# Optimization experiments

Measured on AMD Instinct MI355X. Metric: run time of the kernel, lower is better.

The kernel has to match this reference:

```python
import jax, jax.numpy as jnp
import numpy as np

# dMoE config (matches init_kwargs): D=1024, GLU ffn F=2816 (int(2*4096/3) rounded up to 256),
# E=8 experts, top_k=2, erf-GELU activation, normalize_expert_weights=0 (skip), bias added to output.
D = 1024
F = 2816
E = 8
TOP_K = 2


def setup_inputs() -> dict:
    key = jax.random.key(0)
    ks = jax.random.split(key, 6)
    std = 0.02
    x = jax.random.normal(ks[0], (2, 2048, D), dtype=jnp.float32)
    router_w = jax.random.normal(ks[1], (D, E), dtype=jnp.float32) * std
    w1 = jax.random.normal(ks[2], (E, D, F), dtype=jnp.float32) * std
    v1 = jax.random.normal(ks[3], (E, D, F), dtype=jnp.float32) * std
    w2 = jax.random.normal(ks[4], (E, F, D), dtype=jnp.float32) * std
    bias = jnp.zeros((D,), dtype=jnp.float32)
    return {"x": x, "router_w": router_w, "w1": w1, "v1": v1, "w2": w2, "bias": bias}


def reference(x, router_w, w1, v1, w2, bias):
    B, S, d = x.shape
    xt = x.reshape(B * S, d)                       # [T, D] tokens
    # Router: linear -> softmax over experts -> top-k (no weight renormalization, p=0).
    scores = jax.nn.softmax(xt @ router_w, axis=-1)          # [T, E]
    expert_weights, expert_idx = jax.lax.top_k(scores, TOP_K)  # [T, k]
    # Dropless MoE == dense per-expert GLU MLP combined with top-k weights
    # (non-selected experts get weight 0, mathematically identical to dispatch/combine).
    h = jax.nn.gelu(jnp.einsum('td,edf->tef', xt, w1), approximate=False) \
        * jnp.einsum('td,edf->tef', xt, v1)                   # [T, E, F]
    y = jnp.einsum('tef,efd->ted', h, w2)                     # [T, E, D]
    yk = jnp.take_along_axis(y, expert_idx[:, :, None], axis=1)  # [T, k, D]
    out = jnp.sum(expert_weights[:, :, None] * yk, axis=1) + bias
    return out.reshape(B, S, d)
```

## Files before the change

kernel.cpp:

```cpp
#include <hip/hip_runtime.h>
#include <hip/hip_bf16.h>
#include <math.h>

#define D_DIM 1024
#define F_DIM 2816
#define E_NUM 8

#define BM 128
#define BK 64

typedef __attribute__((ext_vector_type(4))) float f32x4;
typedef __attribute__((ext_vector_type(8))) short short8;

__device__ __forceinline__ unsigned short f2bf(float f) {
    unsigned u = __float_as_uint(f);
    u = (u + 0x7FFFu + ((u >> 16) & 1u)) >> 16;
    return (unsigned short)u;
}

__device__ __forceinline__ float gelu_erf(float z) {
    return 0.5f * z * (1.0f + erff(z * 0.70710678118654752f));
}

__device__ __forceinline__ int swz(int row, int kb) {
    return row * 128 + (kb ^ ((row & 7) << 4));
}

__device__ __forceinline__ uint4 pack8(const unsigned short* h) {
    uint4 r;
    r.x = (unsigned)h[0] | ((unsigned)h[1] << 16);
    r.y = (unsigned)h[2] | ((unsigned)h[3] << 16);
    r.z = (unsigned)h[4] | ((unsigned)h[5] << 16);
    r.w = (unsigned)h[6] | ((unsigned)h[7] << 16);
    return r;
}

__device__ __forceinline__ void gload16(const void* g, void* l) {
    __builtin_amdgcn_global_load_lds(
        (const __attribute__((address_space(1))) unsigned int*)g,
        (__attribute__((address_space(3))) unsigned int*)l,
        16, 0, 0);
}

__global__ __launch_bounds__(256) void transpose_cvt2_kernel(
    const float* __restrict__ srcA, unsigned short* __restrict__ dstA,
    const float* __restrict__ srcB, unsigned short* __restrict__ dstB,
    int R, int C)
{
    __shared__ float tile[64][65];
    int z = blockIdx.z;
    const float* s = (z < E_NUM ? srcA : srcB);
    unsigned short* d = (z < E_NUM ? dstA : dstB);
    int e = z & 7;
    s += (size_t)e * R * C;
    d += (size_t)e * R * C;
    int c0 = blockIdx.x * 64;
    int r0 = blockIdx.y * 64;
    int tid = threadIdx.x;
#pragma unroll
    for (int i = 0; i < 4; ++i) {
        int idx = tid + 256 * i;
        int r = idx >> 4, cc = (idx & 15) * 4;
        float4 v = *(const float4*)(s + (size_t)(r0 + r) * C + c0 + cc);
        tile[r][cc] = v.x; tile[r][cc + 1] = v.y; tile[r][cc + 2] = v.z; tile[r][cc + 3] = v.w;
    }
    __syncthreads();
#pragma unroll
    for (int i = 0; i < 2; ++i) {
        int idx = tid + 256 * i;
        int c = idx >> 3, rr = (idx & 7) * 8;
        unsigned short h[8];
#pragma unroll
        for (int j = 0; j < 8; ++j) h[j] = f2bf(tile[rr + j][c]);
        *(uint4*)(d + (size_t)(c0 + c) * R + r0 + rr) = pack8(h);
    }
}

__global__ __launch_bounds__(256) void transpose_cvt_kernel(
    const float* __restrict__ src, unsigned short* __restrict__ dst, int R, int C)
{
    __shared__ float tile[64][65];
    int e = blockIdx.z;
    const float* s = src + (size_t)e * R * C;
    unsigned short* d = dst + (size_t)e * R * C;
    int c0 = blockIdx.x * 64;
    int r0 = blockIdx.y * 64;
    int tid = threadIdx.x;
#pragma unroll
    for (int i = 0; i < 4; ++i) {
        int idx = tid + 256 * i;
        int r = idx >> 4, cc = (idx & 15) * 4;
        float4 v = *(const float4*)(s + (size_t)(r0 + r) * C + c0 + cc);
        tile[r][cc] = v.x; tile[r][cc + 1] = v.y; tile[r][cc + 2] = v.z; tile[r][cc + 3] = v.w;
    }
    __syncthreads();
#pragma unroll
    for (int i = 0; i < 2; ++i) {
        int idx = tid + 256 * i;
        int c = idx >> 3, rr = (idx & 7) * 8;
        unsigned short h[8];
#pragma unroll
        for (int j = 0; j < 8; ++j) h[j] = f2bf(tile[rr + j][c]);
        *(uint4*)(d + (size_t)(c0 + c) * R + r0 + rr) = pack8(h);
    }
}

__global__ __launch_bounds__(64) void router_kernel(
    const float* __restrict__ x, const float* __restrict__ rw,
    unsigned short* __restrict__ xbf, int* __restrict__ tk_idx,
    float* __restrict__ tk_w, int* __restrict__ counts)
{
    int t = blockIdx.x;
    int lane = threadIdx.x;
    const float* xr = x + (size_t)t * D_DIM;
    float acc[E_NUM];
#pragma unroll
    for (int e = 0; e < E_NUM; ++e) acc[e] = 0.f;
#pragma unroll
    for (int i = 0; i < D_DIM / 64; ++i) {
        int d = lane + 64 * i;
        float xv = xr[d];
        xbf[(size_t)t * D_DIM + d] = f2bf(xv);
        const float* rp = rw + (size_t)d * E_NUM;
#pragma unroll
        for (int e = 0; e < E_NUM; ++e) acc[e] += xv * rp[e];
    }
#pragma unroll
    for (int e = 0; e < E_NUM; ++e) {
#pragma unroll
        for (int s = 32; s > 0; s >>= 1) acc[e] += __shfl_xor(acc[e], s, 64);
    }
    float mx = acc[0];
#pragma unroll
    for (int e = 1; e < E_NUM; ++e) mx = fmaxf(mx, acc[e]);
    float p[E_NUM], se = 0.f;
#pragma unroll
    for (int e = 0; e < E_NUM; ++e) { p[e] = expf(acc[e] - mx); se += p[e]; }
    float inv = 1.f / se;
    int e1 = 0;
#pragma unroll
    for (int e = 1; e < E_NUM; ++e) if (p[e] > p[e1]) e1 = e;
    int e2 = (e1 == 0) ? 1 : 0;
#pragma unroll
    for (int e = 0; e < E_NUM; ++e) if (e != e1 && p[e] > p[e2]) e2 = e;
    if (lane == 0) {
        tk_idx[2 * t] = e1; tk_idx[2 * t + 1] = e2;
        tk_w[2 * t] = p[e1] * inv; tk_w[2 * t + 1] = p[e2] * inv;
        atomicAdd(&counts[e1], 1);
        atomicAdd(&counts[e2], 1);
    }
}

__global__ void scan_kernel(const int* __restrict__ counts, int* __restrict__ offsets,
                            int* __restrict__ cursor,
                            int* __restrict__ tile_e, int* __restrict__ tile_row,
                            int* __restrict__ n_mt)
{
    if (threadIdx.x != 0) return;
    int off = 0, nt = 0;
    for (int e = 0; e < E_NUM; ++e) {
        offsets[e] = off;
        cursor[e] = off;
        int ne = counts[e];
        int nti = (ne + BM - 1) / BM;
        for (int i = 0; i < nti; ++i) { tile_e[nt] = e; tile_row[nt] = off + i * BM; ++nt; }
        off += ne;
    }
    offsets[E_NUM] = off;
    *n_mt = nt;
}

__global__ __launch_bounds__(256) void assign_kernel(
    const int* __restrict__ tk_idx, int* __restrict__ cursor,
    int* __restrict__ pair_token, int* __restrict__ pair_pos, int T)
{
    int t = blockIdx.x * 256 + threadIdx.x;
    if (t >= T) return;
#pragma unroll
    for (int s = 0; s < 2; ++s) {
        int e = tk_idx[2 * t + s];
        int pos = atomicAdd(&cursor[e], 1);
        pair_token[pos] = t;
        pair_pos[2 * t + s] = pos;
    }
}

__global__ __launch_bounds__(512) void gemm1_glu_kernel(
    const unsigned short* __restrict__ xbf,
    const unsigned short* __restrict__ w1t, const unsigned short* __restrict__ v1t,
    const int* __restrict__ pair_token, const int* __restrict__ offsets,
    const int* __restrict__ tile_e, const int* __restrict__ tile_row,
    const int* __restrict__ n_mt,
    unsigned short* __restrict__ hbf)
{
    __shared__ __align__(16) unsigned short As[BM * BK];
    __shared__ __align__(16) unsigned short Bs[256 * BK];

    int flat = blockIdx.x + gridDim.x * blockIdx.y;
    int nwg = gridDim.x * gridDim.y;
    int L = (flat & 7) * (nwg >> 3) + (flat >> 3);
    int mt = L % gridDim.x;
    int strip = L / gridDim.x;
    if (mt >= *n_mt) return;
    int e = tile_e[mt];
    int row0 = tile_row[mt];
    int end = offsets[e + 1];
    int n0 = strip * 128;

    int tid = threadIdx.x;
    int lane = tid & 63;
    int wid = tid >> 6;
    int wr = wid >> 2, wc = wid & 3;
    int sub = lane >> 3;
    int srcoff = (((lane & 7) ^ sub) << 4);

    const unsigned short* W0 = w1t + (size_t)e * D_DIM * F_DIM;
    const unsigned short* W1 = v1t + (size_t)e * D_DIM * F_DIM;

    const char* aptr[2];
#pragma unroll
    for (int i = 0; i < 2; ++i) {
        int r = (wid * 2 + i) * 8 + sub;
        int p = row0 + r;
        if (p >= end) p = end - 1;
        aptr[i] = (const char*)(xbf + (size_t)pair_token[p] * D_DIM) + srcoff;
    }
    const char* bptr[4];
#pragma unroll
    for (int i = 0; i < 4; ++i) {
        int r = (wid * 4 + i) * 8 + sub;
        int s = (r >> 5) & 1;
        int col = n0 + (r >> 6) * 32 + (r & 31);
        const unsigned short* base = s ? W1 : W0;
        bptr[i] = (const char*)(base + (size_t)col * D_DIM) + srcoff;
    }

    f32x4 acc[4][4];
#pragma unroll
    for (int m = 0; m < 4; ++m)
#pragma unroll
        for (int n = 0; n < 4; ++n) acc[m][n] = (f32x4){0.f, 0.f, 0.f, 0.f};

    auto STAGE = [&]() {
#pragma unroll
        for (int i = 0; i < 2; ++i) {
            gload16(aptr[i], (char*)As + (wid * 2 + i) * 1024);
            aptr[i] += 128;
        }
#pragma unroll
        for (int i = 0; i < 4; ++i) {
            gload16(bptr[i], (char*)Bs + (wid * 4 + i) * 1024);
            bptr[i] += 128;
        }
    };

    const int NT = D_DIM / BK;
    for (int kt = 0; kt < NT; ++kt) {
        STAGE();
        __syncthreads();
#pragma unroll
        for (int kk = 0; kk < 2; ++kk) {
            int kb = kk * 64 + (lane >> 4) * 16;
            short8 af[4], bf[4];
#pragma unroll
            for (int m = 0; m < 4; ++m) {
                int row = wr * 64 + m * 16 + (lane & 15);
                af[m] = *(const short8*)((char*)As + swz(row, kb));
            }
#pragma unroll
            for (int n = 0; n < 4; ++n) {
                int rn = wc * 64 + n * 16 + (lane & 15);
                bf[n] = *(const short8*)((char*)Bs + swz(rn, kb));
            }
#pragma unroll
            for (int m = 0; m < 4; ++m)
#pragma unroll
                for (int n = 0; n < 4; ++n)
                    acc[m][n] = __builtin_amdgcn_mfma_f32_16x16x32_bf16(af[m], bf[n], acc[m][n], 0, 0, 0);
        }
        __syncthreads();
    }
#pragma unroll
    for (int m = 0; m < 4; ++m) {
#pragma unroll
        for (int j = 0; j < 4; ++j) {
            int rl = wr * 64 + m * 16 + (lane >> 4) * 4 + j;
            int p = row0 + rl;
            if (p < end) {
#pragma unroll
                for (int n = 0; n < 2; ++n) {
                    float z1 = acc[m][n][j];
                    float z2 = acc[m][n + 2][j];
                    int col = n0 + wc * 32 + n * 16 + (lane & 15);
                    hbf[(size_t)p * F_DIM + col] = f2bf(gelu_erf(z1) * z2);
                }
            }
        }
    }
}

__global__ __launch_bounds__(512) void gemm2_kernel(
    const unsigned short* __restrict__ hbf,
    const unsigned short* __restrict__ w2t,
    const int* __restrict__ offsets,
    const int* __restrict__ tile_e, const int* __restrict__ tile_row,
    const int* __restrict__ n_mt,
    float* __restrict__ ypair)
{
    __shared__ __align__(16) unsigned short As[BM * BK];
    __shared__ __align__(16) unsigned short Bs[256 * BK];

    int flat = blockIdx.x + gridDim.x * blockIdx.y;
    int nwg = gridDim.x * gridDim.y;
    int L = (flat & 7) * (nwg >> 3) + (flat >> 3);
    int mt = L % gridDim.x;
    int strip = L / gridDim.x;
    if (mt >= *n_mt) return;
    int e = tile_e[mt];
    int row0 = tile_row[mt];
    int end = offsets[e + 1];
    int n0 = strip * 256;

    int tid = threadIdx.x;
    int lane = tid & 63;
    int wid = tid >> 6;
    int wr = wid >> 2, wc = wid & 3;
    int sub = lane >> 3;
    int srcoff = (((lane & 7) ^ sub) << 4);

    const unsigned short* W = w2t + (size_t)e * D_DIM * F_DIM;

    const char* aptr[2];
#pragma unroll
    for (int i = 0; i < 2; ++i) {
        int r = (wid * 2 + i) * 8 + sub;
        int p = row0 + r;
        if (p >= end) p = end - 1;
        aptr[i] = (const char*)(hbf + (size_t)p * F_DIM) + srcoff;
    }
    const char* bptr[4];
#pragma unroll
    for (int i = 0; i < 4; ++i) {
        int n = (wid * 4 + i) * 8 + sub;
        bptr[i] = (const char*)(W + (size_t)(n0 + n) * F_DIM) + srcoff;
    }

    f32x4 acc[4][4];
#pragma unroll
    for (int m = 0; m < 4; ++m)
#pragma unroll
        for (int n = 0; n < 4; ++n) acc[m][n] = (f32x4){0.f, 0.f, 0.f, 0.f};

    auto STAGE = [&]() {
#pragma unroll
        for (int i = 0; i < 2; ++i) {
            gload16(aptr[i], (char*)As + (wid * 2 + i) * 1024);
            aptr[i] += 128;
        }
#pragma unroll
        for (int i = 0; i < 4; ++i) {
            gload16(bptr[i], (char*)Bs + (wid * 4 + i) * 1024);
            bptr[i] += 128;
        }
    };

    const int NT = F_DIM / BK;
    for (int kt = 0; kt < NT; ++kt) {
        STAGE();
        __syncthreads();
#pragma unroll
        for (int kk = 0; kk < 2; ++kk) {
            int kb = kk * 64 + (lane >> 4) * 16;
            short8 af[4], bf[4];
#pragma unroll
            for (int m = 0; m < 4; ++m) {
                int row = wr * 64 + m * 16 + (lane & 15);
                af[m] = *(const short8*)((char*)As + swz(row, kb));
            }
#pragma unroll
            for (int n = 0; n < 4; ++n) {
                int rn = wc * 64 + n * 16 + (lane & 15);
                bf[n] = *(const short8*)((char*)Bs + swz(rn, kb));
            }
#pragma unroll
            for (int m = 0; m < 4; ++m)
#pragma unroll
                for (int n = 0; n < 4; ++n)
                    acc[m][n] = __builtin_amdgcn_mfma_f32_16x16x32_bf16(af[m], bf[n], acc[m][n], 0, 0, 0);
        }
        __syncthreads();
    }
#pragma unroll
    for (int m = 0; m < 4; ++m) {
#pragma unroll
        for (int j = 0; j < 4; ++j) {
            int rl = wr * 64 + m * 16 + (lane >> 4) * 4 + j;
            int p = row0 + rl;
            if (p < end) {
#pragma unroll
                for (int n = 0; n < 4; ++n)
                    ypair[(size_t)p * D_DIM + n0 + wc * 64 + n * 16 + (lane & 15)] = acc[m][n][j];
            }
        }
    }
}

__global__ __launch_bounds__(256) void combine_kernel(
    const float* __restrict__ ypair, const int* __restrict__ pair_pos,
    const float* __restrict__ tk_w, const float* __restrict__ bias,
    float* __restrict__ out, int total)
{
    int idx = blockIdx.x * 256 + threadIdx.x;
    if (idx >= total) return;
    int t = idx >> 10;
    int d = idx & (D_DIM - 1);
    int p0 = pair_pos[2 * t], p1 = pair_pos[2 * t + 1];
    float r = bias[d] + tk_w[2 * t] * ypair[(size_t)p0 * D_DIM + d]
                      + tk_w[2 * t + 1] * ypair[(size_t)p1 * D_DIM + d];
    out[idx] = r;
}

__global__ void ws_too_small_kernel(float* out, int n) {
    int i = blockIdx.x * 256 + threadIdx.x;
    if (i < n) out[i] = 12345.0f;
}

extern "C" void kernel_launch(void* const* d_in, const int* in_sizes, int n_in,
                              void* d_out, int out_size, void* d_ws, size_t ws_size,
                              hipStream_t stream) {
    const float* x    = (const float*)d_in[0];
    const float* rw   = (const float*)d_in[1];
    const float* w1   = (const float*)d_in[2];
    const float* v1   = (const float*)d_in[3];
    const float* w2   = (const float*)d_in[4];
    const float* bias = (const float*)d_in[5];
    float* out = (float*)d_out;

    int T = in_sizes[0] / D_DIM;
    int P = 2 * T;
    int maxMT = P / BM + E_NUM;

    char* p = (char*)d_ws;
    char* ws_end = p + ws_size;
    auto alloc = [&](size_t bytes) {
        char* r = p;
        p += (bytes + 255) & ~(size_t)255;
        return r;
    };
    unsigned short* xbf   = (unsigned short*)alloc((size_t)T * D_DIM * 2);
    int*   tk_idx     = (int*)alloc((size_t)T * 2 * 4);
    float* tk_w       = (float*)alloc((size_t)T * 2 * 4);
    int*   counts     = (int*)alloc(E_NUM * 4);
    int*   offsets    = (int*)alloc((E_NUM + 1) * 4);
    int*   cursor     = (int*)alloc(E_NUM * 4);
    int*   tile_e     = (int*)alloc(maxMT * 4);
    int*   tile_row   = (int*)alloc(maxMT * 4);
    int*   n_mt       = (int*)alloc(4);
    int*   pair_token = (int*)alloc((size_t)P * 4);
    int*   pair_pos   = (int*)alloc((size_t)P * 4);
    unsigned short* hbf = (unsigned short*)alloc((size_t)P * F_DIM * 2);
    float* ypair      = (float*)alloc((size_t)P * D_DIM * 4);
    unsigned short* w1t = (unsigned short*)alloc((size_t)E_NUM * D_DIM * F_DIM * 2);
    unsigned short* v1t = (unsigned short*)alloc((size_t)E_NUM * D_DIM * F_DIM * 2);
    unsigned short* w2t = (unsigned short*)alloc((size_t)E_NUM * D_DIM * F_DIM * 2);

    if (p > ws_end) {
        ws_too_small_kernel<<<(out_size + 255) / 256, 256, 0, stream>>>(out, out_size);
        return;
    }

    hipMemsetAsync(counts, 0, E_NUM * 4, stream);
    transpose_cvt2_kernel<<<dim3(F_DIM / 64, D_DIM / 64, 2 * E_NUM), 256, 0, stream>>>(
        w1, w1t, v1, v1t, D_DIM, F_DIM);
    transpose_cvt_kernel<<<dim3(D_DIM / 64, F_DIM / 64, E_NUM), 256, 0, stream>>>(w2, w2t, F_DIM, D_DIM);
    router_kernel<<<T, 64, 0, stream>>>(x, rw, xbf, tk_idx, tk_w, counts);
    scan_kernel<<<1, 64, 0, stream>>>(counts, offsets, cursor, tile_e, tile_row, n_mt);
    assign_kernel<<<(T + 255) / 256, 256, 0, stream>>>(tk_idx, cursor, pair_token, pair_pos, T);
    gemm1_glu_kernel<<<dim3(maxMT, F_DIM / 128), 512, 0, stream>>>(
        xbf, w1t, v1t, pair_token, offsets, tile_e, tile_row, n_mt, hbf);
    gemm2_kernel<<<dim3(maxMT, D_DIM / 256), 512, 0, stream>>>(
        hbf, w2t, offsets, tile_e, tile_row, n_mt, ypair);
    combine_kernel<<<(T * D_DIM + 255) / 256, 256, 0, stream>>>(
        ypair, pair_pos, tk_w, bias, out, T * D_DIM);
}
```

Before: 441.7 us.

## Shrink gemm2 tile to 128 columns, vectorize combine, batch router tokens

gemm2 now uses 256-thread blocks with a 128x128 output tile instead of 128x256, which doubles the grid in N so more workgroups are available to fill CUs. The combine kernel processes four floats per thread with float4 loads and stores. The router now handles four tokens per 256-thread block instead of one per 64-thread block. The smaller gemm2 tile lowers reuse of the staged A tile and reloads hbf twice as often.

```diff
diff --git a/kernel.cpp b/kernel.cpp
--- a/kernel.cpp
+++ b/kernel.cpp
@@ -105,13 +105,13 @@
     }
 }
 
-__global__ __launch_bounds__(64) void router_kernel(
+__global__ __launch_bounds__(256) void router_kernel(
     const float* __restrict__ x, const float* __restrict__ rw,
     unsigned short* __restrict__ xbf, int* __restrict__ tk_idx,
     float* __restrict__ tk_w, int* __restrict__ counts)
 {
-    int t = blockIdx.x;
-    int lane = threadIdx.x;
+    int t = blockIdx.x * 4 + (threadIdx.x >> 6);
+    int lane = threadIdx.x & 63;
     const float* xr = x + (size_t)t * D_DIM;
     float acc[E_NUM];
 #pragma unroll
@@ -299,7 +299,7 @@
     }
 }
 
-__global__ __launch_bounds__(512) void gemm2_kernel(
+__global__ __launch_bounds__(256) void gemm2_kernel(
     const unsigned short* __restrict__ hbf,
     const unsigned short* __restrict__ w2t,
     const int* __restrict__ offsets,
@@ -308,7 +308,7 @@
     float* __restrict__ ypair)
 {
     __shared__ __align__(16) unsigned short As[BM * BK];
-    __shared__ __align__(16) unsigned short Bs[256 * BK];
+    __shared__ __align__(16) unsigned short Bs[128 * BK];
 
     int flat = blockIdx.x + gridDim.x * blockIdx.y;
     int nwg = gridDim.x * gridDim.y;
@@ -319,21 +319,21 @@
     int e = tile_e[mt];
     int row0 = tile_row[mt];
     int end = offsets[e + 1];
-    int n0 = strip * 256;
+    int n0 = strip * 128;
 
     int tid = threadIdx.x;
     int lane = tid & 63;
     int wid = tid >> 6;
-    int wr = wid >> 2, wc = wid & 3;
+    int wr = wid >> 1, wc = wid & 1;
     int sub = lane >> 3;
     int srcoff = (((lane & 7) ^ sub) << 4);
 
     const unsigned short* W = w2t + (size_t)e * D_DIM * F_DIM;
 
-    const char* aptr[2];
-#pragma unroll
-    for (int i = 0; i < 2; ++i) {
-        int r = (wid * 2 + i) * 8 + sub;
+    const char* aptr[4];
+#pragma unroll
+    for (int i = 0; i < 4; ++i) {
+        int r = (wid * 4 + i) * 8 + sub;
         int p = row0 + r;
         if (p >= end) p = end - 1;
         aptr[i] = (const char*)(hbf + (size_t)p * F_DIM) + srcoff;
@@ -353,12 +353,9 @@
 
     auto STAGE = [&]() {
 #pragma unroll
-        for (int i = 0; i < 2; ++i) {
-            gload16(aptr[i], (char*)As + (wid * 2 + i) * 1024);
+        for (int i = 0; i < 4; ++i) {
+            gload16(aptr[i], (char*)As + (wid * 4 + i) * 1024);
             aptr[i] += 128;
-        }
-#pragma unroll
-        for (int i = 0; i < 4; ++i) {
             gload16(bptr[i], (char*)Bs + (wid * 4 + i) * 1024);
             bptr[i] += 128;
         }
@@ -408,16 +405,23 @@
 __global__ __launch_bounds__(256) void combine_kernel(
     const float* __restrict__ ypair, const int* __restrict__ pair_pos,
     const float* __restrict__ tk_w, const float* __restrict__ bias,
-    float* __restrict__ out, int total)
+    float* __restrict__ out, int total4)
 {
     int idx = blockIdx.x * 256 + threadIdx.x;
-    if (idx >= total) return;
-    int t = idx >> 10;
-    int d = idx & (D_DIM - 1);
+    if (idx >= total4) return;
+    int t = idx >> 8;
+    int d4 = idx & 255;
     int p0 = pair_pos[2 * t], p1 = pair_pos[2 * t + 1];
-    float r = bias[d] + tk_w[2 * t] * ypair[(size_t)p0 * D_DIM + d]
-                      + tk_w[2 * t + 1] * ypair[(size_t)p1 * D_DIM + d];
-    out[idx] = r;
+    float w0 = tk_w[2 * t], w1 = tk_w[2 * t + 1];
+    float4 b = ((const float4*)bias)[d4];
+    float4 y0 = ((const float4*)(ypair + (size_t)p0 * D_DIM))[d4];
+    float4 y1 = ((const float4*)(ypair + (size_t)p1 * D_DIM))[d4];
+    float4 r;
+    r.x = b.x + w0 * y0.x + w1 * y1.x;
+    r.y = b.y + w0 * y0.y + w1 * y1.y;
+    r.z = b.z + w0 * y0.z + w1 * y1.z;
+    r.w = b.w + w0 * y0.w + w1 * y1.w;
+    ((float4*)out)[idx] = r;
 }
 
 __global__ void ws_too_small_kernel(float* out, int n) {
@@ -473,13 +477,13 @@
     transpose_cvt2_kernel<<<dim3(F_DIM / 64, D_DIM / 64, 2 * E_NUM), 256, 0, stream>>>(
         w1, w1t, v1, v1t, D_DIM, F_DIM);
     transpose_cvt_kernel<<<dim3(D_DIM / 64, F_DIM / 64, E_NUM), 256, 0, stream>>>(w2, w2t, F_DIM, D_DIM);
-    router_kernel<<<T, 64, 0, stream>>>(x, rw, xbf, tk_idx, tk_w, counts);
+    router_kernel<<<T / 4, 256, 0, stream>>>(x, rw, xbf, tk_idx, tk_w, counts);
     scan_kernel<<<1, 64, 0, stream>>>(counts, offsets, cursor, tile_e, tile_row, n_mt);
     assign_kernel<<<(T + 255) / 256, 256, 0, stream>>>(tk_idx, cursor, pair_token, pair_pos, T);
     gemm1_glu_kernel<<<dim3(maxMT, F_DIM / 128), 512, 0, stream>>>(
         xbf, w1t, v1t, pair_token, offsets, tile_e, tile_row, n_mt, hbf);
-    gemm2_kernel<<<dim3(maxMT, D_DIM / 256), 512, 0, stream>>>(
+    gemm2_kernel<<<dim3(maxMT, D_DIM / 128), 256, 0, stream>>>(
         hbf, w2t, offsets, tile_e, tile_row, n_mt, ypair);
-    combine_kernel<<<(T * D_DIM + 255) / 256, 256, 0, stream>>>(
-        ypair, pair_pos, tk_w, bias, out, T * D_DIM);
-}
+    combine_kernel<<<(T * D_DIM / 4 + 255) / 256, 256, 0, stream>>>(
+        ypair, pair_pos, tk_w, bias, out, T * D_DIM / 4);
+}
```

New measurement: 450.3 us. Within noise of the previous version (+2.0%).
